# Kernel optimization log

Hardware: AMD Instinct MI355X
Metric: run time of the kernel (lower is better)

The kernel has to match this reference:

```python
import jax, jax.numpy as jnp
import numpy as np

B, C, L = 4, 256, 2048
HEADS, DIM_HEAD = 8, 64
HIDDEN = HEADS * DIM_HEAD  # 512


def setup_inputs() -> dict:
    key = jax.random.key(0)
    k1, k2, k3, k4 = jax.random.split(key, 4)
    x = jax.random.normal(k1, (B, C, L), dtype=jnp.float32)
    # Conv1d kernel_size=1 weights, squeezed to [out_ch, in_ch]
    w_qkv = jax.random.normal(k2, (3 * HIDDEN, C), dtype=jnp.float32) * (1.0 / np.sqrt(C))
    w_out = jax.random.normal(k3, (C, HIDDEN), dtype=jnp.float32) * (1.0 / np.sqrt(HIDDEN))
    b_out = jax.random.normal(k4, (C,), dtype=jnp.float32) * 0.01
    return {"x": x, "w_qkv": w_qkv, "w_out": w_out, "b_out": b_out}


def reference(x, w_qkv, w_out, b_out):
    b, c, l = x.shape
    scale = DIM_HEAD ** (-0.5)
    # pointwise conv == channel matmul
    qkv = jnp.einsum('oc,bcl->bol', w_qkv, x)  # [b, 3*hidden, l]
    q, k, v = jnp.split(qkv, 3, axis=1)        # each [b, hidden, l]
    def to_heads(t):
        return t.reshape(b, HEADS, DIM_HEAD, l)  # b h d l
    q, k, v = to_heads(q), to_heads(k), to_heads(v)
    q = q * scale
    sim = jnp.einsum('bhdi,bhdj->bhij', q, k)   # [b,h,l,l]
    attn = jax.nn.softmax(sim, axis=-1)          # stable softmax (max-subtract inside)
    out = jnp.einsum('bhij,bhdj->bhid', attn, v)  # [b,h,l,d]
    out = out.transpose(0, 1, 3, 2).reshape(b, HIDDEN, l)  # b (h d) l
    return jnp.einsum('oc,bcl->bol', w_out, out) + b_out[None, :, None]
```

## Files before the change

kernel.cpp:

```cpp
#include <hip/hip_runtime.h>

typedef unsigned short u16;
typedef unsigned int u32;
typedef __bf16 bf16x8 __attribute__((ext_vector_type(8)));
typedef float f32x4 __attribute__((ext_vector_type(4)));
typedef float f32x8 __attribute__((ext_vector_type(8)));
typedef float f32x16 __attribute__((ext_vector_type(16)));

#define MFMA16(a, b, c) __builtin_amdgcn_mfma_f32_16x16x32_bf16((a), (b), (c), 0, 0, 0)
#define MFMA32(a, b, c) __builtin_amdgcn_mfma_f32_32x32x16_bf16((a), (b), (c), 0, 0, 0)

#define Bn 4
#define Cn 256
#define Ln 2048
#define Hn 8
#define Dn 64
#define HID 512
#define SEGELEMS 4194304

__device__ __forceinline__ u16 bf16_rne(float f) {
  u32 u = __builtin_bit_cast(u32, f);
  u += 0x7FFFu + ((u >> 16) & 1u);
  return (u16)(u >> 16);
}

__device__ __forceinline__ unsigned pack2(float a, float b) {
  return (unsigned)bf16_rne(a) | ((unsigned)bf16_rne(b) << 16);
}

__device__ __forceinline__ float bf16_up(u16 v) {
  u32 u = ((u32)v) << 16;
  return __builtin_bit_cast(float, u);
}

__device__ __forceinline__ u32 comb2(u32 a, u32 c, float s) {
  float lo = (bf16_up((u16)(a & 0xFFFF)) + bf16_up((u16)(c & 0xFFFF))) * s;
  float hi = (bf16_up((u16)(a >> 16)) + bf16_up((u16)(c >> 16))) * s;
  return pack2(lo, hi);
}

__device__ __forceinline__ float fast_exp2(float x) {
#if __has_builtin(__builtin_amdgcn_exp2f)
  return __builtin_amdgcn_exp2f(x);
#else
  return exp2f(x);
#endif
}

__device__ __forceinline__ float fast_rcp(float x) {
#if __has_builtin(__builtin_amdgcn_rcpf)
  return __builtin_amdgcn_rcpf(x);
#else
  return 1.0f / x;
#endif
}

__device__ __forceinline__ void async_load16(const u16* g, u16* l) {
  __builtin_amdgcn_global_load_lds(
      (const __attribute__((address_space(1))) void*)g,
      (__attribute__((address_space(3))) void*)l, 16, 0, 0);
}

__global__ __launch_bounds__(256) void prep_all(const float* __restrict__ wqkv,
                                                const float* __restrict__ wout,
                                                const float* __restrict__ x,
                                                u16* __restrict__ wq,
                                                u16* __restrict__ wo,
                                                u16* __restrict__ xT) {
  const int t = threadIdx.x;
  if (blockIdx.x < 2048) {
    int i = blockIdx.x * 256 + t;
    const float QSCALE = 0.125f * 1.44269504088896340736f;
    if (i < 3 * HID * Cn) {
      float v = wqkv[i];
      if (i < HID * Cn) v *= QSCALE;
      wq[i] = bf16_rne(v);
    } else {
      int j = i - 3 * HID * Cn;
      wo[j] = bf16_rne(wout[j]);
    }
    return;
  }
  __shared__ u16 tile[64][72];
  int v = blockIdx.x - 2048;
  const int lt = v & 31, ct = (v >> 5) & 3, b = v >> 7;
  const float* xp = x + ((size_t)b * Cn + ct * 64) * Ln + lt * 64;
  for (int pass = 0; pass < 4; ++pass) {
    int c = pass * 16 + (t >> 4);
    int l4 = (t & 15) * 4;
    float4 vf = *(const float4*)(xp + (size_t)c * Ln + l4);
    tile[l4 + 0][c] = bf16_rne(vf.x);
    tile[l4 + 1][c] = bf16_rne(vf.y);
    tile[l4 + 2][c] = bf16_rne(vf.z);
    tile[l4 + 3][c] = bf16_rne(vf.w);
  }
  __syncthreads();
  u16* op = xT + ((size_t)b * Ln + lt * 64) * Cn + ct * 64;
  for (int pass = 0; pass < 2; ++pass) {
    int id = pass * 256 + t;
    int l = id >> 3, c8 = (id & 7) * 8;
    *(uint4*)(op + (size_t)l * Cn + c8) = *(const uint4*)&tile[l][c8];
  }
}

__global__ __launch_bounds__(256, 4) void qkv_gemm(const u16* __restrict__ wq,
                                                   const u16* __restrict__ xT,
                                                   u16* __restrict__ qT,
                                                   u16* __restrict__ kT,
                                                   u16* __restrict__ vv) {
  __shared__ u16 Bs[4096];
  __shared__ u16 Aq[4096];
  __shared__ u16 Ak[4096];
  __shared__ u16 Av[4096];
  const int t = threadIdx.x;
  const int nt = blockIdx.x, head = blockIdx.y, b = blockIdx.z;
  const int n0 = nt * 64, m0 = head * 64;
  const int w = t >> 6, lane = t & 63, q = lane >> 4, ln = lane & 15;

  const u16* Bg = xT + ((size_t)b * Ln + n0) * Cn;
  const u16* AgQ = wq + (size_t)m0 * Cn;
  const u16* AgK = wq + (size_t)(512 + m0) * Cn;
  const u16* AgV = wq + (size_t)(1024 + m0) * Cn;

  f32x4 zf = {0.f, 0.f, 0.f, 0.f};
  f32x4 accQ[4], accK[4], accV[4];
  for (int i = 0; i < 4; ++i) { accQ[i] = zf; accK[i] = zf; accV[i] = zf; }

  const int pr0 = w * 8 + (lane >> 3), pr1 = (4 + w) * 8 + (lane >> 3);
  const int pc0 = (lane & 7) ^ (pr0 & 7), pc1 = (lane & 7) ^ (pr1 & 7);

  for (int kk = 0; kk < 4; ++kk) {
    int k0 = kk * 64;
    async_load16(Bg + (size_t)pr0 * Cn + k0 + pc0 * 8, &Bs[w * 512]);
    async_load16(Bg + (size_t)pr1 * Cn + k0 + pc1 * 8, &Bs[(4 + w) * 512]);
    async_load16(AgQ + (size_t)pr0 * Cn + k0 + pc0 * 8, &Aq[w * 512]);
    async_load16(AgQ + (size_t)pr1 * Cn + k0 + pc1 * 8, &Aq[(4 + w) * 512]);
    async_load16(AgK + (size_t)pr0 * Cn + k0 + pc0 * 8, &Ak[w * 512]);
    async_load16(AgK + (size_t)pr1 * Cn + k0 + pc1 * 8, &Ak[(4 + w) * 512]);
    async_load16(AgV + (size_t)pr0 * Cn + k0 + pc0 * 8, &Av[w * 512]);
    async_load16(AgV + (size_t)pr1 * Cn + k0 + pc1 * 8, &Av[(4 + w) * 512]);
    __syncthreads();
    int ar = w * 16 + ln;
    bf16x8 aq0 = *(const bf16x8*)&Aq[ar * 64 + ((q ^ (ln & 7)) * 8)];
    bf16x8 aq1 = *(const bf16x8*)&Aq[ar * 64 + (((q + 4) ^ (ln & 7)) * 8)];
    bf16x8 ak0 = *(const bf16x8*)&Ak[ar * 64 + ((q ^ (ln & 7)) * 8)];
    bf16x8 ak1 = *(const bf16x8*)&Ak[ar * 64 + (((q + 4) ^ (ln & 7)) * 8)];
    bf16x8 av0 = *(const bf16x8*)&Av[ar * 64 + ((q ^ (ln & 7)) * 8)];
    bf16x8 av1 = *(const bf16x8*)&Av[ar * 64 + (((q + 4) ^ (ln & 7)) * 8)];
    for (int n2 = 0; n2 < 4; ++n2) {
      int br = n2 * 16 + ln;
      bf16x8 b0 = *(const bf16x8*)&Bs[br * 64 + ((q ^ (ln & 7)) * 8)];
      bf16x8 b1 = *(const bf16x8*)&Bs[br * 64 + (((q + 4) ^ (ln & 7)) * 8)];
      accQ[n2] = MFMA16(aq0, b0, accQ[n2]);
      accQ[n2] = MFMA16(aq1, b1, accQ[n2]);
      accK[n2] = MFMA16(ak0, b0, accK[n2]);
      accK[n2] = MFMA16(ak1, b1, accK[n2]);
      accV[n2] = MFMA16(av0, b0, accV[n2]);
      accV[n2] = MFMA16(av1, b1, accV[n2]);
    }
    __syncthreads();
  }

  int od0 = w * 16 + q * 4;
  int cw = od0 >> 3, lo = od0 & 7;
  for (int n2 = 0; n2 < 4; ++n2) {
    int l = n2 * 16 + ln;
    uint2 pk;
    pk.x = pack2(accQ[n2][0], accQ[n2][1]);
    pk.y = pack2(accQ[n2][2], accQ[n2][3]);
    *(uint2*)&Bs[l * 64 + ((cw ^ (l & 7)) * 8) + lo] = pk;
  }
  __syncthreads();
  {
    u16* dst = qT + (((size_t)b * Hn + head) * Ln + n0) * Dn;
    for (int pass = 0; pass < 2; ++pass) {
      int id = pass * 256 + t;
      int l = id >> 3, c = id & 7;
      *(uint4*)(dst + (size_t)l * Dn + c * 8) =
          *(const uint4*)&Bs[l * 64 + ((c ^ (l & 7)) * 8)];
    }
  }
  __syncthreads();
  for (int n2 = 0; n2 < 4; ++n2) {
    int l = n2 * 16 + ln;
    uint2 pk;
    pk.x = pack2(accK[n2][0], accK[n2][1]);
    pk.y = pack2(accK[n2][2], accK[n2][3]);
    *(uint2*)&Bs[l * 64 + ((cw ^ (l & 7)) * 8) + lo] = pk;
  }
  __syncthreads();
  {
    u16* dst = kT + (((size_t)b * Hn + head) * Ln + n0) * Dn;
    for (int pass = 0; pass < 2; ++pass) {
      int id = pass * 256 + t;
      int l = id >> 3, c = id & 7;
      *(uint4*)(dst + (size_t)l * Dn + c * 8) =
          *(const uint4*)&Bs[l * 64 + ((c ^ (l & 7)) * 8)];
    }
  }
  __syncthreads();
  for (int n2 = 0; n2 < 4; ++n2) {
    int l = n2 * 16 + ln;
    int lpm = (l & ~12) | ((l & 4) << 1) | ((l & 8) >> 1);
    int cl = lpm >> 3, lov = lpm & 7;
    for (int r = 0; r < 4; ++r) {
      int od = w * 16 + q * 4 + r;
      Bs[od * 64 + ((cl ^ (od & 7)) * 8) + lov] = bf16_rne(accV[n2][r]);
    }
  }
  __syncthreads();
  {
    u16* dst = vv + ((size_t)b * HID + head * 64) * Ln + n0;
    for (int pass = 0; pass < 2; ++pass) {
      int id = pass * 256 + t;
      int od = id >> 3, c = id & 7;
      *(uint4*)(dst + (size_t)od * Ln + c * 8) =
          *(const uint4*)&Bs[od * 64 + ((c ^ (od & 7)) * 8)];
    }
  }
}

__global__ __launch_bounds__(256, 4) void attention(const u16* __restrict__ qT,
                                                    const u16* __restrict__ kT,
                                                    const u16* __restrict__ vv,
                                                    u16* __restrict__ pO,
                                                    float* __restrict__ lP) {
  __shared__ u16 Kt[4096];
  __shared__ u16 Vt[4096];
  const int t = threadIdx.x;
  const int qb = blockIdx.x, bh = blockIdx.y, seg = blockIdx.z;
  const int b = bh >> 3, hh = bh & 7;
  const int w = t >> 6, lane = t & 63;
  const int li = lane & 31, h = lane >> 5;
  const int i0 = qb * 128 + w * 32;

  bf16x8 qf0, qf1, qf2, qf3;
  {
    const u16* qrow = qT + (((size_t)bh) * Ln + i0 + li) * Dn + h * 8;
    qf0 = *(const bf16x8*)(qrow + 0);
    qf1 = *(const bf16x8*)(qrow + 16);
    qf2 = *(const bf16x8*)(qrow + 32);
    qf3 = *(const bf16x8*)(qrow + 48);
  }

  const u16* ksrc0 = kT + ((size_t)bh) * Ln * Dn;
  const u16* vsrc0 = vv + ((size_t)b * HID + hh * Dn) * Ln;

  f32x16 z16;
#pragma unroll
  for (int r = 0; r < 16; ++r) z16[r] = 0.f;
  f32x16 o0 = z16, o1 = z16;
  float lp = 0.f;

  const int pr0 = w * 8 + (lane >> 3), pr1 = (4 + w) * 8 + (lane >> 3);
  const int pc0 = (lane & 7) ^ (pr0 & 7), pc1 = (lane & 7) ^ (pr1 & 7);
  const u16* kadr0 = ksrc0 + ((size_t)seg * 1024 + pr0) * Dn + pc0 * 8;
  const u16* kadr1 = ksrc0 + ((size_t)seg * 1024 + pr1) * Dn + pc1 * 8;
  const u16* vadr0 = vsrc0 + (size_t)pr0 * Ln + seg * 1024 + pc0 * 8;
  const u16* vadr1 = vsrc0 + (size_t)pr1 * Ln + seg * 1024 + pc1 * 8;

  const int sw = (li & 7);

#define LOADKV(jt, K0, K1, V0, V1)                              \
  {                                                             \
    int j0_ = (jt) * 64;                                        \
    K0 = *(const uint4*)(kadr0 + (size_t)j0_ * Dn);             \
    K1 = *(const uint4*)(kadr1 + (size_t)j0_ * Dn);             \
    V0 = *(const uint4*)(vadr0 + j0_);                          \
    V1 = *(const uint4*)(vadr1 + j0_);                          \
  }
#define STOREKV(K0, K1, V0, V1)                                 \
  {                                                             \
    *(uint4*)&Kt[w * 512 + lane * 8] = K0;                      \
    *(uint4*)&Kt[(4 + w) * 512 + lane * 8] = K1;                \
    *(uint4*)&Vt[w * 512 + lane * 8] = V0;                      \
    *(uint4*)&Vt[(4 + w) * 512 + lane * 8] = V1;                \
  }

#define COMPUTE()                                                              \
  {                                                                            \
    f32x16 sv0, sv1;                                                           \
    {                                                                          \
      bf16x8 k0 = *(const bf16x8*)&Kt[li * 64 + (((0 + h) ^ sw) * 8)];         \
      bf16x8 k1 = *(const bf16x8*)&Kt[(32 + li) * 64 + (((0 + h) ^ sw) * 8)];  \
      sv0 = MFMA32(k0, qf0, z16);                                              \
      sv1 = MFMA32(k1, qf0, z16);                                              \
    }                                                                          \
    {                                                                          \
      bf16x8 k0 = *(const bf16x8*)&Kt[li * 64 + (((2 + h) ^ sw) * 8)];         \
      bf16x8 k1 = *(const bf16x8*)&Kt[(32 + li) * 64 + (((2 + h) ^ sw) * 8)];  \
      sv0 = MFMA32(k0, qf1, sv0);                                              \
      sv1 = MFMA32(k1, qf1, sv1);                                              \
    }                                                                          \
    {                                                                          \
      bf16x8 k0 = *(const bf16x8*)&Kt[li * 64 + (((4 + h) ^ sw) * 8)];         \
      bf16x8 k1 = *(const bf16x8*)&Kt[(32 + li) * 64 + (((4 + h) ^ sw) * 8)];  \
      sv0 = MFMA32(k0, qf2, sv0);                                              \
      sv1 = MFMA32(k1, qf2, sv1);                                              \
    }                                                                          \
    {                                                                          \
      bf16x8 k0 = *(const bf16x8*)&Kt[li * 64 + (((6 + h) ^ sw) * 8)];         \
      bf16x8 k1 = *(const bf16x8*)&Kt[(32 + li) * 64 + (((6 + h) ^ sw) * 8)];  \
      sv0 = MFMA32(k0, qf3, sv0);                                              \
      sv1 = MFMA32(k1, qf3, sv1);                                              \
    }                                                                          \
    _Pragma("unroll") for (int g = 0; g < 16; ++g) {                           \
      sv0[g] = fast_exp2(sv0[g]);                                              \
      sv1[g] = fast_exp2(sv1[g]);                                              \
      lp += sv0[g] + sv1[g];                                                   \
    }                                                                          \
    f32x8 e0 = __builtin_shufflevector(sv0, sv0, 0, 1, 2, 3, 4, 5, 6, 7);      \
    f32x8 e1 = __builtin_shufflevector(sv0, sv0, 8, 9, 10, 11, 12, 13, 14, 15);\
    f32x8 e2 = __builtin_shufflevector(sv1, sv1, 0, 1, 2, 3, 4, 5, 6, 7);      \
    f32x8 e3 = __builtin_shufflevector(sv1, sv1, 8, 9, 10, 11, 12, 13, 14, 15);\
    bf16x8 pf0 = __builtin_convertvector(e0, bf16x8);                          \
    bf16x8 pf1 = __builtin_convertvector(e1, bf16x8);                          \
    bf16x8 pf2 = __builtin_convertvector(e2, bf16x8);                          \
    bf16x8 pf3 = __builtin_convertvector(e3, bf16x8);                          \
    _Pragma("unroll") for (int jc = 0; jc < 4; ++jc) {                         \
      int ch = 2 * jc + h;                                                     \
      bf16x8 pf = (jc == 0) ? pf0 : (jc == 1) ? pf1 : (jc == 2) ? pf2 : pf3;   \
      bf16x8 vf0 = *(const bf16x8*)&Vt[li * 64 + ((ch ^ sw) * 8)];             \
      bf16x8 vf1 = *(const bf16x8*)&Vt[(32 + li) * 64 + ((ch ^ sw) * 8)];      \
      o0 = MFMA32(pf, vf0, o0);                                                \
      o1 = MFMA32(pf, vf1, o1);                                                \
    }                                                                          \
  }

  uint4 ka0, ka1, va0, va1, kb0, kb1, vb0, vb1;
  LOADKV(0, ka0, ka1, va0, va1);
  for (int jt = 0; jt < 16; jt += 2) {
    if (jt) __syncthreads();
    STOREKV(ka0, ka1, va0, va1);
    __syncthreads();
    LOADKV(jt + 1, kb0, kb1, vb0, vb1);
    COMPUTE();
    __syncthreads();
    STOREKV(kb0, kb1, vb0, vb1);
    __syncthreads();
    if (jt + 2 < 16) LOADKV(jt + 2, ka0, ka1, va0, va1);
    COMPUTE();
  }
#undef LOADKV
#undef STOREKV
#undef COMPUTE

  float lsum = lp + __shfl_xor(lp, 32);
  if (h == 0)
    lP[(((size_t)seg * Bn + b) * Hn + hh) * Ln + i0 + li] = lsum;
  u16* po = pO + (size_t)seg * SEGELEMS;
#pragma unroll
  for (int r = 0; r < 16; ++r) {
    int ir = (r & 3) + 8 * (r >> 2) + 4 * h;
    size_t base = ((size_t)b * Ln + i0 + ir) * HID + hh * Dn + li;
    po[base] = bf16_rne(o0[r]);
    po[base + 32] = bf16_rne(o1[r]);
  }
}

__global__ __launch_bounds__(256, 4) void out_gemm(const u16* __restrict__ wo,
                                                   const u16* __restrict__ pO,
                                                   const float* __restrict__ lP,
                                                   const float* __restrict__ bout,
                                                   float* __restrict__ out) {
  __shared__ u16 As[4096];
  __shared__ u16 Bs[2048];
  const int t = threadIdx.x;
  const int nt = blockIdx.x, mt = blockIdx.y, b = blockIdx.z;
  const int m0 = mt * 64, n0 = nt * 32;
  const int w = t >> 6, lane = t & 63, q = lane >> 4, ln = lane & 15;

  const u16* Ag = wo + (size_t)m0 * HID;

  f32x4 zf = {0.f, 0.f, 0.f, 0.f};
  f32x4 acc[2];
  acc[0] = zf; acc[1] = zf;

  const int pr0 = w * 8 + (lane >> 3), pr1 = (4 + w) * 8 + (lane >> 3);
  const int pc0 = (lane & 7) ^ (pr0 & 7), pc1 = (lane & 7) ^ (pr1 & 7);
  const u16* Aad0 = Ag + (size_t)pr0 * HID + pc0 * 8;
  const u16* Aad1 = Ag + (size_t)pr1 * HID + pc1 * 8;
  const int irow = n0 + pr0;
  const u16* Bs0 = pO + ((size_t)b * Ln + irow) * HID + pc0 * 8;
  const u16* Bs1 = Bs0 + SEGELEMS;
  const float* lp0 = lP + (size_t)b * Hn * Ln + irow;
  const float* lp1 = lP + (size_t)(Bn + b) * Hn * Ln + irow;

#define LOADAB(kk, A0, A1, U0, U1, L0, L1)       \
  {                                              \
    int k0_ = (kk) * 64;                         \
    A0 = *(const uint4*)(Aad0 + k0_);            \
    A1 = *(const uint4*)(Aad1 + k0_);            \
    U0 = *(const uint4*)(Bs0 + k0_);             \
    U1 = *(const uint4*)(Bs1 + k0_);             \
    L0 = lp0[(size_t)(kk) * Ln];                 \
    L1 = lp1[(size_t)(kk) * Ln];                 \
  }
#define STOREAB(A0, A1, U0, U1, L0, L1)          \
  {                                              \
    float s_ = fast_rcp(L0 + L1);                \
    uint4 Bc_;                                   \
    Bc_.x = comb2(U0.x, U1.x, s_);               \
    Bc_.y = comb2(U0.y, U1.y, s_);               \
    Bc_.z = comb2(U0.z, U1.z, s_);               \
    Bc_.w = comb2(U0.w, U1.w, s_);               \
    *(uint4*)&As[w * 512 + lane * 8] = A0;       \
    *(uint4*)&As[(4 + w) * 512 + lane * 8] = A1; \
    *(uint4*)&Bs[w * 512 + lane * 8] = Bc_;      \
  }
#define COMPUTEC()                                                             \
  {                                                                            \
    int ar = w * 16 + ln;                                                      \
    bf16x8 a0 = *(const bf16x8*)&As[ar * 64 + ((q ^ (ln & 7)) * 8)];           \
    bf16x8 a1 = *(const bf16x8*)&As[ar * 64 + (((q + 4) ^ (ln & 7)) * 8)];     \
    for (int n2 = 0; n2 < 2; ++n2) {                                           \
      int br = n2 * 16 + ln;                                                   \
      bf16x8 b0 = *(const bf16x8*)&Bs[br * 64 + ((q ^ (ln & 7)) * 8)];         \
      bf16x8 b1 = *(const bf16x8*)&Bs[br * 64 + (((q + 4) ^ (ln & 7)) * 8)];   \
      acc[n2] = MFMA16(a0, b0, acc[n2]);                                       \
      acc[n2] = MFMA16(a1, b1, acc[n2]);                                       \
    }                                                                          \
  }

  uint4 aa0, aa1, ua0, ua1, ab0, ab1, ub0, ub1;
  float la0, la1, lb0, lb1;
  LOADAB(0, aa0, aa1, ua0, ua1, la0, la1);
  for (int kk = 0; kk < 8; kk += 2) {
    if (kk) __syncthreads();
    STOREAB(aa0, aa1, ua0, ua1, la0, la1);
    __syncthreads();
    LOADAB(kk + 1, ab0, ab1, ub0, ub1, lb0, lb1);
    COMPUTEC();
    __syncthreads();
    STOREAB(ab0, ab1, ub0, ub1, lb0, lb1);
    __syncthreads();
    if (kk + 2 < 8) LOADAB(kk + 2, aa0, aa1, ua0, ua1, la0, la1);
    COMPUTEC();
  }
#undef LOADAB
#undef STOREAB
#undef COMPUTEC

  float bias[4];
  for (int r = 0; r < 4; ++r) bias[r] = bout[m0 + w * 16 + q * 4 + r];
  for (int n2 = 0; n2 < 2; ++n2) {
    int l = n0 + n2 * 16 + ln;
    for (int r = 0; r < 4; ++r) {
      int o = m0 + w * 16 + q * 4 + r;
      out[((size_t)b * Cn + o) * Ln + l] = acc[n2][r] + bias[r];
    }
  }
}

extern "C" void kernel_launch(void* const* d_in, const int* in_sizes, int n_in,
                              void* d_out, int out_size, void* d_ws, size_t ws_size,
                              hipStream_t stream) {
  const float* x = (const float*)d_in[0];
  const float* wqkv = (const float*)d_in[1];
  const float* wout = (const float*)d_in[2];
  const float* bout = (const float*)d_in[3];
  float* out = (float*)d_out;
  char* ws = (char*)d_ws;

  u16* wq_b  = (u16*)(ws + 0);
  u16* wo_b  = (u16*)(ws + 786432);
  float* lP  = (float*)(ws + 1048576);
  u16* qT    = (u16*)(ws + 1572864);
  u16* kT    = (u16*)(ws + 9961472);
  u16* vv    = (u16*)(ws + 18350080);
  u16* xT    = (u16*)(ws + 26738688);
  u16* pO    = (u16*)(ws + 26738688);

  prep_all<<<2560, 256, 0, stream>>>(wqkv, wout, x, wq_b, wo_b, xT);
  qkv_gemm<<<dim3(32, 8, 4), 256, 0, stream>>>(wq_b, xT, qT, kT, vv);
  attention<<<dim3(16, 32, 2), 256, 0, stream>>>(qT, kT, vv, pO, lP);
  out_gemm<<<dim3(64, 4, 4), 256, 0, stream>>>(wo_b, pO, lP, bout, out);
}
```

Baseline: 164.3 us.

## Double-buffer LDS tiles with async global-to-LDS loads in QKV GEMM and attention

Both the QKV projection GEMM and the attention kernel now use two LDS buffers per tile. The next K-chunk (or K/V tile) is issued with async global-to-LDS loads while the current buffer is being computed on. In attention this replaces the register-staged load/store pattern, cutting the barriers per tile from two to one and freeing the staging registers. The cost is twice the LDS per block (64KB for qkv_gemm), which could lower occupancy, and correctness depends on async_load16 completion being ordered by the barrier.

Result: faster. 136.4 us (-17.0%).

```diff
diff --git a/kernel.cpp b/kernel.cpp
--- a/kernel.cpp
+++ b/kernel.cpp
@@ -108,10 +108,10 @@
                                                    u16* __restrict__ qT,
                                                    u16* __restrict__ kT,
                                                    u16* __restrict__ vv) {
-  __shared__ u16 Bs[4096];
-  __shared__ u16 Aq[4096];
-  __shared__ u16 Ak[4096];
-  __shared__ u16 Av[4096];
+  __shared__ u16 Bs[2][4096];
+  __shared__ u16 Aq[2][4096];
+  __shared__ u16 Ak[2][4096];
+  __shared__ u16 Av[2][4096];
   const int t = threadIdx.x;
   const int nt = blockIdx.x, head = blockIdx.y, b = blockIdx.z;
   const int n0 = nt * 64, m0 = head * 64;
@@ -129,38 +129,54 @@
   const int pr0 = w * 8 + (lane >> 3), pr1 = (4 + w) * 8 + (lane >> 3);
   const int pc0 = (lane & 7) ^ (pr0 & 7), pc1 = (lane & 7) ^ (pr1 & 7);
 
-  for (int kk = 0; kk < 4; ++kk) {
-    int k0 = kk * 64;
-    async_load16(Bg + (size_t)pr0 * Cn + k0 + pc0 * 8, &Bs[w * 512]);
-    async_load16(Bg + (size_t)pr1 * Cn + k0 + pc1 * 8, &Bs[(4 + w) * 512]);
-    async_load16(AgQ + (size_t)pr0 * Cn + k0 + pc0 * 8, &Aq[w * 512]);
-    async_load16(AgQ + (size_t)pr1 * Cn + k0 + pc1 * 8, &Aq[(4 + w) * 512]);
-    async_load16(AgK + (size_t)pr0 * Cn + k0 + pc0 * 8, &Ak[w * 512]);
-    async_load16(AgK + (size_t)pr1 * Cn + k0 + pc1 * 8, &Ak[(4 + w) * 512]);
-    async_load16(AgV + (size_t)pr0 * Cn + k0 + pc0 * 8, &Av[w * 512]);
-    async_load16(AgV + (size_t)pr1 * Cn + k0 + pc1 * 8, &Av[(4 + w) * 512]);
-    __syncthreads();
-    int ar = w * 16 + ln;
-    bf16x8 aq0 = *(const bf16x8*)&Aq[ar * 64 + ((q ^ (ln & 7)) * 8)];
-    bf16x8 aq1 = *(const bf16x8*)&Aq[ar * 64 + (((q + 4) ^ (ln & 7)) * 8)];
-    bf16x8 ak0 = *(const bf16x8*)&Ak[ar * 64 + ((q ^ (ln & 7)) * 8)];
-    bf16x8 ak1 = *(const bf16x8*)&Ak[ar * 64 + (((q + 4) ^ (ln & 7)) * 8)];
-    bf16x8 av0 = *(const bf16x8*)&Av[ar * 64 + ((q ^ (ln & 7)) * 8)];
-    bf16x8 av1 = *(const bf16x8*)&Av[ar * 64 + (((q + 4) ^ (ln & 7)) * 8)];
-    for (int n2 = 0; n2 < 4; ++n2) {
-      int br = n2 * 16 + ln;
-      bf16x8 b0 = *(const bf16x8*)&Bs[br * 64 + ((q ^ (ln & 7)) * 8)];
-      bf16x8 b1 = *(const bf16x8*)&Bs[br * 64 + (((q + 4) ^ (ln & 7)) * 8)];
-      accQ[n2] = MFMA16(aq0, b0, accQ[n2]);
-      accQ[n2] = MFMA16(aq1, b1, accQ[n2]);
-      accK[n2] = MFMA16(ak0, b0, accK[n2]);
-      accK[n2] = MFMA16(ak1, b1, accK[n2]);
-      accV[n2] = MFMA16(av0, b0, accV[n2]);
-      accV[n2] = MFMA16(av1, b1, accV[n2]);
-    }
-    __syncthreads();
-  }
-
+#define QISSUE(kk, db)                                                      \
+  {                                                                         \
+    int k0_ = (kk) * 64;                                                    \
+    async_load16(Bg + (size_t)pr0 * Cn + k0_ + pc0 * 8, &Bs[db][w * 512]);  \
+    async_load16(Bg + (size_t)pr1 * Cn + k0_ + pc1 * 8, &Bs[db][(4 + w) * 512]); \
+    async_load16(AgQ + (size_t)pr0 * Cn + k0_ + pc0 * 8, &Aq[db][w * 512]); \
+    async_load16(AgQ + (size_t)pr1 * Cn + k0_ + pc1 * 8, &Aq[db][(4 + w) * 512]); \
+    async_load16(AgK + (size_t)pr0 * Cn + k0_ + pc0 * 8, &Ak[db][w * 512]); \
+    async_load16(AgK + (size_t)pr1 * Cn + k0_ + pc1 * 8, &Ak[db][(4 + w) * 512]); \
+    async_load16(AgV + (size_t)pr0 * Cn + k0_ + pc0 * 8, &Av[db][w * 512]); \
+    async_load16(AgV + (size_t)pr1 * Cn + k0_ + pc1 * 8, &Av[db][(4 + w) * 512]); \
+  }
+#define QCOMPUTE(db)                                                           \
+  {                                                                            \
+    int ar = w * 16 + ln;                                                      \
+    bf16x8 aq0 = *(const bf16x8*)&Aq[db][ar * 64 + ((q ^ (ln & 7)) * 8)];      \
+    bf16x8 aq1 = *(const bf16x8*)&Aq[db][ar * 64 + (((q + 4) ^ (ln & 7)) * 8)];\
+    bf16x8 ak0 = *(const bf16x8*)&Ak[db][ar * 64 + ((q ^ (ln & 7)) * 8)];      \
+    bf16x8 ak1 = *(const bf16x8*)&Ak[db][ar * 64 + (((q + 4) ^ (ln & 7)) * 8)];\
+    bf16x8 av0 = *(const bf16x8*)&Av[db][ar * 64 + ((q ^ (ln & 7)) * 8)];      \
+    bf16x8 av1 = *(const bf16x8*)&Av[db][ar * 64 + (((q + 4) ^ (ln & 7)) * 8)];\
+    for (int n2 = 0; n2 < 4; ++n2) {                                           \
+      int br = n2 * 16 + ln;                                                   \
+      bf16x8 b0 = *(const bf16x8*)&Bs[db][br * 64 + ((q ^ (ln & 7)) * 8)];     \
+      bf16x8 b1 = *(const bf16x8*)&Bs[db][br * 64 + (((q + 4) ^ (ln & 7)) * 8)];\
+      accQ[n2] = MFMA16(aq0, b0, accQ[n2]);                                    \
+      accQ[n2] = MFMA16(aq1, b1, accQ[n2]);                                    \
+      accK[n2] = MFMA16(ak0, b0, accK[n2]);                                    \
+      accK[n2] = MFMA16(ak1, b1, accK[n2]);                                    \
+      accV[n2] = MFMA16(av0, b0, accV[n2]);                                    \
+      accV[n2] = MFMA16(av1, b1, accV[n2]);                                    \
+    }                                                                          \
+  }
+
+  QISSUE(0, 0);
+  __syncthreads();
+  for (int kk = 0; kk < 4; kk += 2) {
+    if (kk + 1 < 4) QISSUE(kk + 1, 1);
+    QCOMPUTE(0);
+    __syncthreads();
+    if (kk + 2 < 4) QISSUE(kk + 2, 0);
+    QCOMPUTE(1);
+    __syncthreads();
+  }
+#undef QISSUE
+#undef QCOMPUTE
+
+  u16* Rs = Bs[0];
   int od0 = w * 16 + q * 4;
   int cw = od0 >> 3, lo = od0 & 7;
   for (int n2 = 0; n2 < 4; ++n2) {
@@ -168,7 +184,7 @@
     uint2 pk;
     pk.x = pack2(accQ[n2][0], accQ[n2][1]);
     pk.y = pack2(accQ[n2][2], accQ[n2][3]);
-    *(uint2*)&Bs[l * 64 + ((cw ^ (l & 7)) * 8) + lo] = pk;
+    *(uint2*)&Rs[l * 64 + ((cw ^ (l & 7)) * 8) + lo] = pk;
   }
   __syncthreads();
   {
@@ -177,7 +193,7 @@
       int id = pass * 256 + t;
       int l = id >> 3, c = id & 7;
       *(uint4*)(dst + (size_t)l * Dn + c * 8) =
-          *(const uint4*)&Bs[l * 64 + ((c ^ (l & 7)) * 8)];
+          *(const uint4*)&Rs[l * 64 + ((c ^ (l & 7)) * 8)];
     }
   }
   __syncthreads();
@@ -186,7 +202,7 @@
     uint2 pk;
     pk.x = pack2(accK[n2][0], accK[n2][1]);
     pk.y = pack2(accK[n2][2], accK[n2][3]);
-    *(uint2*)&Bs[l * 64 + ((cw ^ (l & 7)) * 8) + lo] = pk;
+    *(uint2*)&Rs[l * 64 + ((cw ^ (l & 7)) * 8) + lo] = pk;
   }
   __syncthreads();
   {
@@ -195,7 +211,7 @@
       int id = pass * 256 + t;
       int l = id >> 3, c = id & 7;
       *(uint4*)(dst + (size_t)l * Dn + c * 8) =
-          *(const uint4*)&Bs[l * 64 + ((c ^ (l & 7)) * 8)];
+          *(const uint4*)&Rs[l * 64 + ((c ^ (l & 7)) * 8)];
     }
   }
   __syncthreads();
@@ -205,7 +221,7 @@
     int cl = lpm >> 3, lov = lpm & 7;
     for (int r = 0; r < 4; ++r) {
       int od = w * 16 + q * 4 + r;
-      Bs[od * 64 + ((cl ^ (od & 7)) * 8) + lov] = bf16_rne(accV[n2][r]);
+      Rs[od * 64 + ((cl ^ (od & 7)) * 8) + lov] = bf16_rne(accV[n2][r]);
     }
   }
   __syncthreads();
@@ -215,7 +231,7 @@
       int id = pass * 256 + t;
       int od = id >> 3, c = id & 7;
       *(uint4*)(dst + (size_t)od * Ln + c * 8) =
-          *(const uint4*)&Bs[od * 64 + ((c ^ (od & 7)) * 8)];
+          *(const uint4*)&Rs[od * 64 + ((c ^ (od & 7)) * 8)];
     }
   }
 }
@@ -225,8 +241,8 @@
                                                     const u16* __restrict__ vv,
                                                     u16* __restrict__ pO,
                                                     float* __restrict__ lP) {
-  __shared__ u16 Kt[4096];
-  __shared__ u16 Vt[4096];
+  __shared__ u16 Kt[2][4096];
+  __shared__ u16 Vt[2][4096];
   const int t = threadIdx.x;
   const int qb = blockIdx.x, bh = blockIdx.y, seg = blockIdx.z;
   const int b = bh >> 3, hh = bh & 7;
@@ -259,48 +275,41 @@
   const u16* vadr0 = vsrc0 + (size_t)pr0 * Ln + seg * 1024 + pc0 * 8;
   const u16* vadr1 = vsrc0 + (size_t)pr1 * Ln + seg * 1024 + pc1 * 8;
 
-  const int sw = (li & 7);
-
-#define LOADKV(jt, K0, K1, V0, V1)                              \
+  const int sw = li & 7;
+
+#define ISSUE(jt, db)                                           \
   {                                                             \
     int j0_ = (jt) * 64;                                        \
-    K0 = *(const uint4*)(kadr0 + (size_t)j0_ * Dn);             \
-    K1 = *(const uint4*)(kadr1 + (size_t)j0_ * Dn);             \
-    V0 = *(const uint4*)(vadr0 + j0_);                          \
-    V1 = *(const uint4*)(vadr1 + j0_);                          \
-  }
-#define STOREKV(K0, K1, V0, V1)                                 \
-  {                                                             \
-    *(uint4*)&Kt[w * 512 + lane * 8] = K0;                      \
-    *(uint4*)&Kt[(4 + w) * 512 + lane * 8] = K1;                \
-    *(uint4*)&Vt[w * 512 + lane * 8] = V0;                      \
-    *(uint4*)&Vt[(4 + w) * 512 + lane * 8] = V1;                \
-  }
-
-#define COMPUTE()                                                              \
+    async_load16(kadr0 + (size_t)j0_ * Dn, &Kt[db][w * 512]);   \
+    async_load16(kadr1 + (size_t)j0_ * Dn, &Kt[db][(4 + w) * 512]); \
+    async_load16(vadr0 + j0_, &Vt[db][w * 512]);                \
+    async_load16(vadr1 + j0_, &Vt[db][(4 + w) * 512]);          \
+  }
+
+#define COMPUTE(db)                                                            \
   {                                                                            \
     f32x16 sv0, sv1;                                                           \
     {                                                                          \
-      bf16x8 k0 = *(const bf16x8*)&Kt[li * 64 + (((0 + h) ^ sw) * 8)];         \
-      bf16x8 k1 = *(const bf16x8*)&Kt[(32 + li) * 64 + (((0 + h) ^ sw) * 8)];  \
+      bf16x8 k0 = *(const bf16x8*)&Kt[db][li * 64 + (((0 + h) ^ sw) * 8)];     \
+      bf16x8 k1 = *(const bf16x8*)&Kt[db][(32 + li) * 64 + (((0 + h) ^ sw) * 8)]; \
       sv0 = MFMA32(k0, qf0, z16);                                              \
       sv1 = MFMA32(k1, qf0, z16);                                              \
     }                                                                          \
     {                                                                          \
-      bf16x8 k0 = *(const bf16x8*)&Kt[li * 64 + (((2 + h) ^ sw) * 8)];         \
-      bf16x8 k1 = *(const bf16x8*)&Kt[(32 + li) * 64 + (((2 + h) ^ sw) * 8)];  \
+      bf16x8 k0 = *(const bf16x8*)&Kt[db][li * 64 + (((2 + h) ^ sw) * 8)];     \
+      bf16x8 k1 = *(const bf16x8*)&Kt[db][(32 + li) * 64 + (((2 + h) ^ sw) * 8)]; \
       sv0 = MFMA32(k0, qf1, sv0);                                              \
       sv1 = MFMA32(k1, qf1, sv1);                                              \
     }                                                                          \
     {                                                                          \
-      bf16x8 k0 = *(const bf16x8*)&Kt[li * 64 + (((4 + h) ^ sw) * 8)];         \
-      bf16x8 k1 = *(const bf16x8*)&Kt[(32 + li) * 64 + (((4 + h) ^ sw) * 8)];  \
+      bf16x8 k0 = *(const bf16x8*)&Kt[db][li * 64 + (((4 + h) ^ sw) * 8)];     \
+      bf16x8 k1 = *(const bf16x8*)&Kt[db][(32 + li) * 64 + (((4 + h) ^ sw) * 8)]; \
       sv0 = MFMA32(k0, qf2, sv0);                                              \
       sv1 = MFMA32(k1, qf2, sv1);                                              \
     }                                                                          \
     {                                                                          \
-      bf16x8 k0 = *(const bf16x8*)&Kt[li * 64 + (((6 + h) ^ sw) * 8)];         \
-      bf16x8 k1 = *(const bf16x8*)&Kt[(32 + li) * 64 + (((6 + h) ^ sw) * 8)];  \
+      bf16x8 k0 = *(const bf16x8*)&Kt[db][li * 64 + (((6 + h) ^ sw) * 8)];     \
+      bf16x8 k1 = *(const bf16x8*)&Kt[db][(32 + li) * 64 + (((6 + h) ^ sw) * 8)]; \
       sv0 = MFMA32(k0, qf3, sv0);                                              \
       sv1 = MFMA32(k1, qf3, sv1);                                              \
     }                                                                          \
@@ -309,40 +318,35 @@
       sv1[g] = fast_exp2(sv1[g]);                                              \
       lp += sv0[g] + sv1[g];                                                   \
     }                                                                          \
-    f32x8 e0 = __builtin_shufflevector(sv0, sv0, 0, 1, 2, 3, 4, 5, 6, 7);      \
-    f32x8 e1 = __builtin_shufflevector(sv0, sv0, 8, 9, 10, 11, 12, 13, 14, 15);\
-    f32x8 e2 = __builtin_shufflevector(sv1, sv1, 0, 1, 2, 3, 4, 5, 6, 7);      \
-    f32x8 e3 = __builtin_shufflevector(sv1, sv1, 8, 9, 10, 11, 12, 13, 14, 15);\
-    bf16x8 pf0 = __builtin_convertvector(e0, bf16x8);                          \
-    bf16x8 pf1 = __builtin_convertvector(e1, bf16x8);                          \
-    bf16x8 pf2 = __builtin_convertvector(e2, bf16x8);                          \
-    bf16x8 pf3 = __builtin_convertvector(e3, bf16x8);                          \
+    bf16x8 pf0 = __builtin_convertvector(                                      \
+        __builtin_shufflevector(sv0, sv0, 0, 1, 2, 3, 4, 5, 6, 7), bf16x8);    \
+    bf16x8 pf1 = __builtin_convertvector(                                      \
+        __builtin_shufflevector(sv0, sv0, 8, 9, 10, 11, 12, 13, 14, 15), bf16x8); \
+    bf16x8 pf2 = __builtin_convertvector(                                      \
+        __builtin_shufflevector(sv1, sv1, 0, 1, 2, 3, 4, 5, 6, 7), bf16x8);    \
+    bf16x8 pf3 = __builtin_convertvector(                                      \
+        __builtin_shufflevector(sv1, sv1, 8, 9, 10, 11, 12, 13, 14, 15), bf16x8); \
     _Pragma("unroll") for (int jc = 0; jc < 4; ++jc) {                         \
       int ch = 2 * jc + h;                                                     \
       bf16x8 pf = (jc == 0) ? pf0 : (jc == 1) ? pf1 : (jc == 2) ? pf2 : pf3;   \
-      bf16x8 vf0 = *(const bf16x8*)&Vt[li * 64 + ((ch ^ sw) * 8)];             \
-      bf16x8 vf1 = *(const bf16x8*)&Vt[(32 + li) * 64 + ((ch ^ sw) * 8)];      \
+      bf16x8 vf0 = *(const bf16x8*)&Vt[db][li * 64 + ((ch ^ sw) * 8)];         \
+      bf16x8 vf1 = *(const bf16x8*)&Vt[db][(32 + li) * 64 + ((ch ^ sw) * 8)];  \
       o0 = MFMA32(pf, vf0, o0);                                                \
       o1 = MFMA32(pf, vf1, o1);                                                \
     }                                                                          \
   }
 
-  uint4 ka0, ka1, va0, va1, kb0, kb1, vb0, vb1;
-  LOADKV(0, ka0, ka1, va0, va1);
+  ISSUE(0, 0);
+  __syncthreads();
   for (int jt = 0; jt < 16; jt += 2) {
-    if (jt) __syncthreads();
-    STOREKV(ka0, ka1, va0, va1);
-    __syncthreads();
-    LOADKV(jt + 1, kb0, kb1, vb0, vb1);
-    COMPUTE();
-    __syncthreads();
-    STOREKV(kb0, kb1, vb0, vb1);
-    __syncthreads();
-    if (jt + 2 < 16) LOADKV(jt + 2, ka0, ka1, va0, va1);
-    COMPUTE();
-  }
-#undef LOADKV
-#undef STOREKV
+    if (jt + 1 < 16) ISSUE(jt + 1, 1);
+    COMPUTE(0);
+    __syncthreads();
+    if (jt + 2 < 16) ISSUE(jt + 2, 0);
+    COMPUTE(1);
+    __syncthreads();
+  }
+#undef ISSUE
 #undef COMPUTE
 
   float lsum = lp + __shfl_xor(lp, 32);
```
